# Optimization experiments

Measured on AMD Instinct MI355X. Metric: run time of the kernel, lower is better.

Reference implementation:

```python
import jax, jax.numpy as jnp
import numpy as np
import math

N_HEAD = 16
HEAD_QKV = 1024  # total qkv width; head_dim = HEAD_QKV // N_HEAD
WM_DECAY_LENGTH = 2048
WM_DECAY_RATE = 1.0
WM_ECHOIC = 16


def decay_weight_matrix(n):
    # power_law decay, faithful to get_decay_weight_matrix
    dl = WM_DECAY_LENGTH - WM_ECHOIC + 1
    nums = jnp.linspace(0.0, 1.0, dl)
    decay_values = 1.0 - jnp.power(nums, 1.0 / (np.e * WM_DECAY_RATE))
    decay_values = jnp.concatenate([jnp.ones(WM_ECHOIC - 1), decay_values])  # [WM_DECAY_LENGTH]
    decay_values = decay_values[:n]
    idx = jnp.arange(n)[:, None] - jnp.arange(n)[None, :]  # [n,n], negative above diag
    mat = decay_values[jnp.clip(idx, 0, n - 1)]
    return jnp.tril(mat).astype(jnp.float32)


def setup_inputs() -> dict:
    key = jax.random.key(0)
    k1, k2, k3 = jax.random.split(key, 3)
    B, T, C = 2, 2048, 1024
    x = jax.random.normal(k1, (B, T, C), dtype=jnp.float32)
    W_attn = jax.random.normal(k2, (C, 3 * HEAD_QKV), dtype=jnp.float32) * (1.0 / math.sqrt(C))
    W_proj = jax.random.normal(k3, (HEAD_QKV, C), dtype=jnp.float32) * (1.0 / math.sqrt(HEAD_QKV))
    return {"x": x, "W_attn": W_attn, "W_proj": W_proj}


def reference(x, W_attn, W_proj):
    B, T, C = x.shape
    hd = HEAD_QKV // N_HEAD
    qkv = x @ W_attn  # [B,T,3*HEAD_QKV]
    q, k, v = jnp.split(qkv, 3, axis=-1)
    # [B,T,HQKV] -> [B,H,T,hd]
    q = q.reshape(B, T, N_HEAD, hd).transpose(0, 2, 1, 3)
    k = k.reshape(B, T, N_HEAD, hd).transpose(0, 2, 1, 3)
    v = v.reshape(B, T, N_HEAD, hd).transpose(0, 2, 1, 3)
    att = jnp.einsum('bhqd,bhkd->bhqk', q, k) * (1.0 / math.sqrt(hd))
    causal = jnp.tril(jnp.ones((T, T), dtype=bool))
    att = jnp.where(causal, att, -jnp.inf)
    att = jax.nn.softmax(att, axis=-1)
    att = att * decay_weight_matrix(T)  # post-softmax multiplicative decay
    y = jnp.einsum('bhqk,bhkd->bhqd', att, v)
    y = y.transpose(0, 2, 1, 3).reshape(B, T, HEAD_QKV)
    return y @ W_proj
```

## Files before the change

kernel.cpp:

```cpp
#include <hip/hip_runtime.h>
#include <math.h>

#define B_  2
#define T_  2048
#define C_  1024
#define NH_ 16
#define HD_ 64
#define N3_ 3072

typedef float f32x4 __attribute__((ext_vector_type(4)));
typedef short bf16x8 __attribute__((ext_vector_type(8)));
typedef unsigned short u16;
typedef float f32x4_base __attribute__((ext_vector_type(4)));
typedef f32x4_base __attribute__((aligned(4))) f32x4u;

#define QSCALE 0.18033688011112042f

#if __has_builtin(__builtin_amdgcn_exp2f)
#define EXP2(x) __builtin_amdgcn_exp2f(x)
#else
#define EXP2(x) exp2f(x)
#endif

__device__ __forceinline__ u16 f2bf(float x) {
  unsigned int u = __builtin_bit_cast(unsigned int, x);
  u += 0x7FFFu + ((u >> 16) & 1u);
  return (u16)(u >> 16);
}

__device__ __forceinline__ unsigned int cvt_pk_bf16(float lo, float hi) {
  unsigned int r;
  asm("v_cvt_pk_bf16_f32 %0, %1, %2" : "=v"(r) : "v"(lo), "v"(hi));
  return r;
}

#define GLD16(g, l) __builtin_amdgcn_global_load_lds( \
    (__attribute__((address_space(1))) void*)(g), \
    (__attribute__((address_space(3))) void*)(l), 16, 0, 0)

__global__ __launch_bounds__(256) void cvt4_kernel(const float* __restrict__ in,
                                                   u16* __restrict__ out, int n) {
  int i = (blockIdx.x * 256 + threadIdx.x) * 4;
  if (i >= n) return;
  float4 v = *(const float4*)(in + i);
  ushort4 o;
  o.x = f2bf(v.x); o.y = f2bf(v.y); o.z = f2bf(v.z); o.w = f2bf(v.w);
  *(ushort4*)(out + i) = o;
}

__global__ __launch_bounds__(256) void transpose_cvt_kernel(const float* __restrict__ in,
                                                            u16* __restrict__ out,
                                                            int R, int Cc) {
  __shared__ float tile[32][33];
  int c0 = blockIdx.x * 32, r0 = blockIdx.y * 32;
  int tx = threadIdx.x & 31, ty = threadIdx.x >> 5;
#pragma unroll
  for (int rr = ty; rr < 32; rr += 8)
    tile[rr][tx] = in[(size_t)(r0 + rr) * Cc + c0 + tx];
  __syncthreads();
#pragma unroll
  for (int rr = ty; rr < 32; rr += 8)
    out[(size_t)(c0 + rr) * R + r0 + tx] = f2bf(tile[tx][rr]);
}

__global__ __launch_bounds__(256) void decay_init_kernel(float* __restrict__ decR) {
  int j = blockIdx.x * 256 + threadIdx.x;
  if (j >= 2176) return;
  int d = 2047 - j;
  float v = 1.0f;
  if (d >= 15) v = 1.0f - powf((float)(d - 15) * (1.0f / 2032.0f), 0.36787944117144233f);
  decR[j] = v;
}

__global__ __launch_bounds__(256) void vtrans_kernel(const u16* __restrict__ V,
                                                     u16* __restrict__ VT) {
  __shared__ u16 tile[64][72];
  int bh = blockIdx.y, t0 = blockIdx.x * 64;
  const u16* src = V + ((size_t)bh * T_ + t0) * HD_;
  int r = threadIdx.x >> 2;
  int c8 = (threadIdx.x & 3) * 16;
  *(bf16x8*)(&tile[r][c8])     = *(const bf16x8*)(src + (size_t)r * HD_ + c8);
  *(bf16x8*)(&tile[r][c8 + 8]) = *(const bf16x8*)(src + (size_t)r * HD_ + c8 + 8);
  __syncthreads();
  int d = threadIdx.x >> 2;
  int tc = (threadIdx.x & 3) * 16;
  u16 outv[16];
#pragma unroll
  for (int j = 0; j < 16; ++j) outv[j] = tile[tc + j][d];
  u16* dst = VT + ((size_t)bh * HD_ + d) * T_ + t0 + tc;
  *(bf16x8*)(dst)     = *(bf16x8*)(outv);
  *(bf16x8*)(dst + 8) = *(bf16x8*)(outv + 8);
}

template<int MODE>
__global__ __launch_bounds__(256, 3) void gemm128_kernel(
    const u16* __restrict__ A, const u16* __restrict__ Bt,
    float* __restrict__ Cf, u16* __restrict__ Cq, u16* __restrict__ Vt,
    int M, int N, int K)
{
  __shared__ char lds[32768];
  const int lane = threadIdx.x & 63;
  const int wave = threadIdx.x >> 6;
  const int nxb = N >> 7;
  const int orig = blockIdx.x;
  const int cpx = (int)gridDim.x >> 3;
  const int wg = (orig & 7) * cpx + (orig >> 3);
  const int m0 = (wg / nxb) << 7;
  const int n0 = (wg % nxb) << 7;
  const int wm = wave >> 1, wn = wave & 1;

  f32x4 acc[4][4] = {};

#define GSTAGE(buf, k0)                                                          \
  {                                                                              \
    _Pragma("unroll")                                                            \
    for (int c = 0; c < 2; ++c) {                                                \
      int chunk = wave * 2048 + c * 1024;                                        \
      int row = (chunk >> 6) + (lane >> 2);                                      \
      int wb = ((lane & 3) << 4) ^ ((row & 3) << 4);                             \
      GLD16((const char*)(A  + (size_t)(m0 + row) * K + (k0)) + wb,              \
            lds + (buf) * 16384 + chunk);                                        \
      GLD16((const char*)(Bt + (size_t)(n0 + row) * K + (k0)) + wb,              \
            lds + (buf) * 16384 + 8192 + chunk);                                 \
    }                                                                            \
  }

  GSTAGE(0, 0);
  __syncthreads();

  for (int k0 = 0; k0 < K; k0 += 32) {
    const int cur = (k0 >> 5) & 1;
    if (k0 + 32 < K) GSTAGE(cur ^ 1, k0 + 32);
    const char* base = lds + cur * 16384;
    bf16x8 af[4], bfr[4];
#pragma unroll
    for (int m = 0; m < 4; ++m) {
      int row = wm * 64 + m * 16 + (lane & 15);
      int wb = ((lane >> 4) << 4) ^ ((row & 3) << 4);
      af[m] = *(const bf16x8*)(base + row * 64 + wb);
    }
#pragma unroll
    for (int n = 0; n < 4; ++n) {
      int row = wn * 64 + n * 16 + (lane & 15);
      int wb = ((lane >> 4) << 4) ^ ((row & 3) << 4);
      bfr[n] = *(const bf16x8*)(base + 8192 + row * 64 + wb);
    }
    __builtin_amdgcn_s_setprio(1);
#pragma unroll
    for (int m = 0; m < 4; ++m)
#pragma unroll
      for (int n = 0; n < 4; ++n)
        acc[m][n] = __builtin_amdgcn_mfma_f32_16x16x32_bf16(af[m], bfr[n], acc[m][n], 0, 0, 0);
    __builtin_amdgcn_s_setprio(0);
    __syncthreads();
  }

#pragma unroll
  for (int m = 0; m < 4; ++m) {
    int grow0 = m0 + wm * 64 + m * 16 + ((lane >> 4) << 2);
#pragma unroll
    for (int n = 0; n < 4; ++n) {
      int gcol = n0 + wn * 64 + n * 16 + (lane & 15);
      f32x4 v = acc[m][n];
#pragma unroll
      for (int r = 0; r < 4; ++r) {
        int grow = grow0 + r;
        if (MODE == 0) {
          int bb = grow >> 11, tt = grow & 2047;
          int which = gcol >> 10, rem = gcol & 1023;
          int hh = rem >> 6, dd = rem & 63;
          if (which < 2) {
            float ov = (which == 0) ? v[r] * QSCALE : v[r];
            Cq[((size_t)(which * 32 + bb * 16 + hh) * 2048 + tt) * 64 + dd] = f2bf(ov);
          } else {
            Vt[((size_t)(bb * 16 + hh) * 2048 + tt) * 64 + dd] = f2bf(v[r]);
          }
        } else {
          Cf[(size_t)grow * N + gcol] = v[r];
        }
      }
    }
  }
#undef GSTAGE
}

__global__ __launch_bounds__(256, 3) void attn_kernel(
    const u16* __restrict__ qkb, const u16* __restrict__ vtg,
    const float* __restrict__ decR, u16* __restrict__ yb)
{
  __shared__ char klds[2][8192];
  __shared__ char vlds[2][8192];
  __shared__ u16 plds[128 * 76];

  const int lane = threadIdx.x & 63;
  const int wave = threadIdx.x >> 6;
  const int quad = lane >> 4;
  const int l15 = lane & 15;
  const int orig = blockIdx.x;
  const int wg = ((orig & 7) << 6) + (orig >> 3);
  const int qtA = wg & 15;
  const int qtB = 31 - qtA;
  const int bh = wg >> 4;
  const int b = bh >> 4, h = bh & 15;

  const u16* Q   = qkb + (size_t)bh * T_ * HD_;
  const u16* Kg  = qkb + (size_t)(32 + bh) * T_ * HD_;
  const u16* VTg = vtg + (size_t)bh * HD_ * T_;

  const int wrowB = qtB * 64 + wave * 16;
  const int wrowA = qtA * 64 + wave * 16;
  const int qB = wrowB + l15;
  const int qA = wrowA + l15;
  const int rbase0B = 2047 - qB + quad * 4;
  const int rbase0A = 2047 - qA + quad * 4;

  bf16x8 qaB[2], qaA[2];
  { const u16* qp = Q + (size_t)(wrowB + l15) * HD_ + quad * 8;
    qaB[0] = *(const bf16x8*)qp; qaB[1] = *(const bf16x8*)(qp + 32); }
  { const u16* qp = Q + (size_t)(wrowA + l15) * HD_ + quad * 8;
    qaA[0] = *(const bf16x8*)qp; qaA[1] = *(const bf16x8*)(qp + 32); }

  f32x4 accB[4] = {}, accA[4] = {};
  float lsumB = 0.0f, lsumA = 0.0f;

#define ASTAGE(buf, kt)                                                          \
  {                                                                              \
    _Pragma("unroll")                                                            \
    for (int c = 0; c < 2; ++c) {                                                \
      int chunk = wave * 2048 + c * 1024;                                        \
      int row = (chunk >> 7) + (lane >> 3);                                      \
      int wb = ((lane & 7) << 4) ^ ((row & 7) << 4);                             \
      GLD16((const char*)(Kg + (size_t)((kt) * 64 + row) * HD_) + wb,            \
            klds[buf] + chunk);                                                  \
      GLD16((const char*)(VTg + (size_t)row * T_ + (kt) * 64) + wb,              \
            vlds[buf] + chunk);                                                  \
    }                                                                            \
  }

  ASTAGE(0, 0);
  __syncthreads();

  const int nkt = qtB + 1;
  for (int kt = 0; kt < nkt; ++kt) {
    const int cur = kt & 1;
    if (kt + 1 < nkt) ASTAGE(cur ^ 1, kt + 1);
    const bool actA = (kt <= qtA);

    bf16x8 kf[4][2];
#pragma unroll
    for (int f = 0; f < 4; ++f) {
      int krow = f * 16 + l15;
      int base = krow * 128;
      int msk = (krow & 7) << 4;
      kf[f][0] = *(const bf16x8*)(klds[cur] + base + ((quad * 16) ^ msk));
      kf[f][1] = *(const bf16x8*)(klds[cur] + base + ((64 + quad * 16) ^ msk));
    }

    const float* dRB = decR + (rbase0B + kt * 64);
    const float* dRA = decR + (rbase0A + kt * 64);
    f32x4 dB[4], dA[4];
#pragma unroll
    for (int f = 0; f < 4; ++f) dB[f] = *(const f32x4u*)(dRB + f * 16);
    if (actA) {
#pragma unroll
      for (int f = 0; f < 4; ++f) dA[f] = *(const f32x4u*)(dRA + f * 16);
    }

    f32x4 sB[4], sA[4];
    __builtin_amdgcn_s_setprio(1);
#pragma unroll
    for (int f = 0; f < 4; ++f) {
      f32x4 t = {};
      t = __builtin_amdgcn_mfma_f32_16x16x32_bf16(kf[f][0], qaB[0], t, 0, 0, 0);
      t = __builtin_amdgcn_mfma_f32_16x16x32_bf16(kf[f][1], qaB[1], t, 0, 0, 0);
      sB[f] = t;
    }
    if (actA) {
#pragma unroll
      for (int f = 0; f < 4; ++f) {
        f32x4 t = {};
        t = __builtin_amdgcn_mfma_f32_16x16x32_bf16(kf[f][0], qaA[0], t, 0, 0, 0);
        t = __builtin_amdgcn_mfma_f32_16x16x32_bf16(kf[f][1], qaA[1], t, 0, 0, 0);
        sA[f] = t;
      }
    }
    __builtin_amdgcn_s_setprio(0);

    if (kt == qtB) {
#pragma unroll
      for (int f = 0; f < 4; ++f) {
        int key0 = kt * 64 + f * 16 + quad * 4;
#pragma unroll
        for (int r = 0; r < 4; ++r)
          if (key0 + r > qB) sB[f][r] = -1e30f;
      }
    }
    if (actA && kt == qtA) {
#pragma unroll
      for (int f = 0; f < 4; ++f) {
        int key0 = kt * 64 + f * 16 + quad * 4;
#pragma unroll
        for (int r = 0; r < 4; ++r)
          if (key0 + r > qA) sA[f][r] = -1e30f;
      }
    }

#pragma unroll
    for (int f = 0; f < 4; ++f) {
      f32x4 p;
#pragma unroll
      for (int r = 0; r < 4; ++r) p[r] = EXP2(sB[f][r]);
      lsumB += (p[0] + p[1]) + (p[2] + p[3]);
      unsigned int w0 = cvt_pk_bf16(p[0] * dB[f][0], p[1] * dB[f][1]);
      unsigned int w1 = cvt_pk_bf16(p[2] * dB[f][2], p[3] * dB[f][3]);
      uint2 wv; wv.x = w0; wv.y = w1;
      *(uint2*)(plds + (size_t)(wave * 16 + l15) * 76 + f * 16 + quad * 4) = wv;
    }
    if (actA) {
#pragma unroll
      for (int f = 0; f < 4; ++f) {
        f32x4 p;
#pragma unroll
        for (int r = 0; r < 4; ++r) p[r] = EXP2(sA[f][r]);
        lsumA += (p[0] + p[1]) + (p[2] + p[3]);
        unsigned int w0 = cvt_pk_bf16(p[0] * dA[f][0], p[1] * dA[f][1]);
        unsigned int w1 = cvt_pk_bf16(p[2] * dA[f][2], p[3] * dA[f][3]);
        uint2 wv; wv.x = w0; wv.y = w1;
        *(uint2*)(plds + (size_t)(64 + wave * 16 + l15) * 76 + f * 16 + quad * 4) = wv;
      }
    }

    bf16x8 vf[4][2];
#pragma unroll
    for (int n = 0; n < 4; ++n) {
      int vrow = n * 16 + l15;
      int mskv = (vrow & 7) << 4;
#pragma unroll
      for (int ks = 0; ks < 2; ++ks)
        vf[n][ks] = *(const bf16x8*)(vlds[cur] + vrow * 128 + ((ks * 64 + quad * 16) ^ mskv));
    }

    __builtin_amdgcn_s_setprio(1);
#pragma unroll
    for (int ks = 0; ks < 2; ++ks) {
      bf16x8 pa = *(const bf16x8*)(plds + (size_t)(wave * 16 + l15) * 76 + ks * 32 + quad * 8);
#pragma unroll
      for (int n = 0; n < 4; ++n)
        accB[n] = __builtin_amdgcn_mfma_f32_16x16x32_bf16(pa, vf[n][ks], accB[n], 0, 0, 0);
    }
    if (actA) {
#pragma unroll
      for (int ks = 0; ks < 2; ++ks) {
        bf16x8 pa = *(const bf16x8*)(plds + (size_t)(64 + wave * 16 + l15) * 76 + ks * 32 + quad * 8);
#pragma unroll
        for (int n = 0; n < 4; ++n)
          accA[n] = __builtin_amdgcn_mfma_f32_16x16x32_bf16(pa, vf[n][ks], accA[n], 0, 0, 0);
      }
    }
    __builtin_amdgcn_s_setprio(0);
    __syncthreads();
  }
#undef ASTAGE

  lsumB += __shfl_xor(lsumB, 16); lsumB += __shfl_xor(lsumB, 32);
  lsumA += __shfl_xor(lsumA, 16); lsumA += __shfl_xor(lsumA, 32);
  float rB[4], rA[4];
#pragma unroll
  for (int r = 0; r < 4; ++r) {
    rB[r] = 1.0f / __shfl(lsumB, quad * 4 + r, 16);
    rA[r] = 1.0f / __shfl(lsumA, quad * 4 + r, 16);
  }
#pragma unroll
  for (int n = 0; n < 4; ++n) {
    int d = h * 64 + n * 16 + l15;
#pragma unroll
    for (int r = 0; r < 4; ++r) {
      int tB = wrowB + quad * 4 + r;
      int tA = wrowA + quad * 4 + r;
      yb[((size_t)b * T_ + tB) * 1024 + d] = f2bf(accB[n][r] * rB[r]);
      yb[((size_t)b * T_ + tA) * 1024 + d] = f2bf(accA[n][r] * rA[r]);
    }
  }
}

extern "C" void kernel_launch(void* const* d_in, const int* in_sizes, int n_in,
                              void* d_out, int out_size, void* d_ws, size_t ws_size,
                              hipStream_t stream) {
  const float* x  = (const float*)d_in[0];
  const float* Wa = (const float*)d_in[1];
  const float* Wp = (const float*)d_in[2];
  float* out = (float*)d_out;
  char* ws = (char*)d_ws;

  u16*   xb    = (u16*)(ws + 0);
  u16*   WaT   = (u16*)(ws + 8388608);
  u16*   WpT   = (u16*)(ws + 14680064);
  u16*   qkb   = (u16*)(ws + 16777216);
  u16*   Vtmp  = (u16*)(ws + 33554432);
  u16*   VT    = (u16*)(ws + 41943040);
  float* decR  = (float*)Vtmp;
  u16*   yb    = xb;

  cvt4_kernel<<<4096, 256, 0, stream>>>(x, xb, B_ * T_ * C_);
  transpose_cvt_kernel<<<dim3(96, 32), 256, 0, stream>>>(Wa, WaT, C_, N3_);
  transpose_cvt_kernel<<<dim3(32, 32), 256, 0, stream>>>(Wp, WpT, C_, C_);

  gemm128_kernel<0><<<768, 256, 0, stream>>>(
      xb, WaT, nullptr, qkb, Vtmp, B_ * T_, N3_, C_);
  vtrans_kernel<<<dim3(32, 32), 256, 0, stream>>>(Vtmp, VT);
  decay_init_kernel<<<9, 256, 0, stream>>>(decR);
  attn_kernel<<<512, 256, 0, stream>>>(qkb, VT, decR, yb);
  gemm128_kernel<1><<<256, 256, 0, stream>>>(
      yb, WpT, out, nullptr, nullptr, B_ * T_, 1024, 1024);
}
```

Before: 120.7 us.

## Fuse prep kernels, triple-buffer GEMM, write V transposed, prefetch decay in attention

Combines the x conversion, both weight transposes and the decay table init into one prep kernel, and drops the separate V transpose kernel by having the QKV GEMM epilogue write V directly in transposed layout. The GEMM moves to a three-stage LDS pipeline with explicit vmcnt waits and one barrier per iteration. Attention prefetches the next tile's decay factors into registers, replaces the trailing syncthreads with a barrier at loop top, remaps blocks so heads stay grouped per XCD with balanced query tiles, and lowers launch bounds to 2 waves. This cuts launch count and global round trips but raises LDS and register use, which lowers GEMM occupancy.

```diff
diff --git a/kernel.cpp b/kernel.cpp
--- a/kernel.cpp
+++ b/kernel.cpp
@@ -38,58 +38,49 @@
     (__attribute__((address_space(1))) void*)(g), \
     (__attribute__((address_space(3))) void*)(l), 16, 0, 0)
 
-__global__ __launch_bounds__(256) void cvt4_kernel(const float* __restrict__ in,
-                                                   u16* __restrict__ out, int n) {
-  int i = (blockIdx.x * 256 + threadIdx.x) * 4;
-  if (i >= n) return;
-  float4 v = *(const float4*)(in + i);
-  ushort4 o;
-  o.x = f2bf(v.x); o.y = f2bf(v.y); o.z = f2bf(v.z); o.w = f2bf(v.w);
-  *(ushort4*)(out + i) = o;
-}
-
-__global__ __launch_bounds__(256) void transpose_cvt_kernel(const float* __restrict__ in,
-                                                            u16* __restrict__ out,
-                                                            int R, int Cc) {
+__global__ __launch_bounds__(256) void prep_kernel(
+    const float* __restrict__ x, u16* __restrict__ xb,
+    const float* __restrict__ Wa, u16* __restrict__ WaT,
+    const float* __restrict__ Wp, u16* __restrict__ WpT,
+    float* __restrict__ decR)
+{
   __shared__ float tile[32][33];
-  int c0 = blockIdx.x * 32, r0 = blockIdx.y * 32;
-  int tx = threadIdx.x & 31, ty = threadIdx.x >> 5;
-#pragma unroll
-  for (int rr = ty; rr < 32; rr += 8)
-    tile[rr][tx] = in[(size_t)(r0 + rr) * Cc + c0 + tx];
-  __syncthreads();
-#pragma unroll
-  for (int rr = ty; rr < 32; rr += 8)
-    out[(size_t)(c0 + rr) * R + r0 + tx] = f2bf(tile[tx][rr]);
-}
-
-__global__ __launch_bounds__(256) void decay_init_kernel(float* __restrict__ decR) {
-  int j = blockIdx.x * 256 + threadIdx.x;
-  if (j >= 2176) return;
-  int d = 2047 - j;
-  float v = 1.0f;
-  if (d >= 15) v = 1.0f - powf((float)(d - 15) * (1.0f / 2032.0f), 0.36787944117144233f);
-  decR[j] = v;
-}
-
-__global__ __launch_bounds__(256) void vtrans_kernel(const u16* __restrict__ V,
-                                                     u16* __restrict__ VT) {
-  __shared__ u16 tile[64][72];
-  int bh = blockIdx.y, t0 = blockIdx.x * 64;
-  const u16* src = V + ((size_t)bh * T_ + t0) * HD_;
-  int r = threadIdx.x >> 2;
-  int c8 = (threadIdx.x & 3) * 16;
-  *(bf16x8*)(&tile[r][c8])     = *(const bf16x8*)(src + (size_t)r * HD_ + c8);
-  *(bf16x8*)(&tile[r][c8 + 8]) = *(const bf16x8*)(src + (size_t)r * HD_ + c8 + 8);
-  __syncthreads();
-  int d = threadIdx.x >> 2;
-  int tc = (threadIdx.x & 3) * 16;
-  u16 outv[16];
-#pragma unroll
-  for (int j = 0; j < 16; ++j) outv[j] = tile[tc + j][d];
-  u16* dst = VT + ((size_t)bh * HD_ + d) * T_ + t0 + tc;
-  *(bf16x8*)(dst)     = *(bf16x8*)(outv);
-  *(bf16x8*)(dst + 8) = *(bf16x8*)(outv + 8);
+  const int bid = blockIdx.x;
+  const int tid = threadIdx.x;
+  if (bid < 4096) {
+    int i = (bid * 256 + tid) * 4;
+    float4 v = *(const float4*)(x + i);
+    ushort4 o;
+    o.x = f2bf(v.x); o.y = f2bf(v.y); o.z = f2bf(v.z); o.w = f2bf(v.w);
+    *(ushort4*)(xb + i) = o;
+  } else if (bid < 8192) {
+    const float* in; u16* out; int Cc, c0, r0;
+    if (bid < 7168) {
+      int t = bid - 4096;
+      in = Wa; out = WaT; Cc = N3_;
+      c0 = (t % 96) * 32; r0 = (t / 96) * 32;
+    } else {
+      int t = bid - 7168;
+      in = Wp; out = WpT; Cc = C_;
+      c0 = (t % 32) * 32; r0 = (t / 32) * 32;
+    }
+    int tx = tid & 31, ty = tid >> 5;
+#pragma unroll
+    for (int rr = ty; rr < 32; rr += 8)
+      tile[rr][tx] = in[(size_t)(r0 + rr) * Cc + c0 + tx];
+    __syncthreads();
+#pragma unroll
+    for (int rr = ty; rr < 32; rr += 8)
+      out[(size_t)(c0 + rr) * 1024 + r0 + tx] = f2bf(tile[tx][rr]);
+  } else {
+    int j = (bid - 8192) * 256 + tid;
+    if (j < 4352) {
+      int d = 2047 - j;
+      float v = 1.0f;
+      if (d >= 15) v = 1.0f - powf((float)(d - 15) * (1.0f / 2032.0f), 0.36787944117144233f);
+      decR[j] = v;
+    }
+  }
 }
 
 template<int MODE>
@@ -98,7 +89,7 @@
     float* __restrict__ Cf, u16* __restrict__ Cq, u16* __restrict__ Vt,
     int M, int N, int K)
 {
-  __shared__ char lds[32768];
+  __shared__ char lds[49152];
   const int lane = threadIdx.x & 63;
   const int wave = threadIdx.x >> 6;
   const int nxb = N >> 7;
@@ -125,13 +116,19 @@
     }                                                                            \
   }
 
+  const int nk = K >> 5;
   GSTAGE(0, 0);
+  GSTAGE(1, 32);
   __syncthreads();
 
-  for (int k0 = 0; k0 < K; k0 += 32) {
-    const int cur = (k0 >> 5) & 1;
-    if (k0 + 32 < K) GSTAGE(cur ^ 1, k0 + 32);
-    const char* base = lds + cur * 16384;
+  for (int i = 0; i < nk; ++i) {
+    if (i + 1 < nk) asm volatile("s_waitcnt vmcnt(4)" ::: "memory");
+    else            asm volatile("s_waitcnt vmcnt(0)" ::: "memory");
+    __builtin_amdgcn_s_barrier();
+    __builtin_amdgcn_sched_barrier(0);
+    if (i + 2 < nk) GSTAGE((i + 2) % 3, (i + 2) * 32);
+
+    const char* base = lds + (i % 3) * 16384;
     bf16x8 af[4], bfr[4];
 #pragma unroll
     for (int m = 0; m < 4; ++m) {
@@ -152,7 +149,6 @@
       for (int n = 0; n < 4; ++n)
         acc[m][n] = __builtin_amdgcn_mfma_f32_16x16x32_bf16(af[m], bfr[n], acc[m][n], 0, 0, 0);
     __builtin_amdgcn_s_setprio(0);
-    __syncthreads();
   }
 
 #pragma unroll
@@ -162,29 +158,32 @@
     for (int n = 0; n < 4; ++n) {
       int gcol = n0 + wn * 64 + n * 16 + (lane & 15);
       f32x4 v = acc[m][n];
-#pragma unroll
-      for (int r = 0; r < 4; ++r) {
-        int grow = grow0 + r;
-        if (MODE == 0) {
-          int bb = grow >> 11, tt = grow & 2047;
-          int which = gcol >> 10, rem = gcol & 1023;
-          int hh = rem >> 6, dd = rem & 63;
-          if (which < 2) {
+      if (MODE == 0) {
+        int bb = grow0 >> 11, tt0 = grow0 & 2047;
+        int which = gcol >> 10, rem = gcol & 1023;
+        int hh = rem >> 6, dd = rem & 63;
+        if (which < 2) {
+#pragma unroll
+          for (int r = 0; r < 4; ++r) {
             float ov = (which == 0) ? v[r] * QSCALE : v[r];
-            Cq[((size_t)(which * 32 + bb * 16 + hh) * 2048 + tt) * 64 + dd] = f2bf(ov);
-          } else {
-            Vt[((size_t)(bb * 16 + hh) * 2048 + tt) * 64 + dd] = f2bf(v[r]);
+            Cq[((size_t)(which * 32 + bb * 16 + hh) * 2048 + tt0 + r) * 64 + dd] = f2bf(ov);
           }
         } else {
-          Cf[(size_t)grow * N + gcol] = v[r];
+          ushort4 o;
+          o.x = f2bf(v[0]); o.y = f2bf(v[1]); o.z = f2bf(v[2]); o.w = f2bf(v[3]);
+          *(ushort4*)(Vt + ((size_t)(bb * 16 + hh) * 64 + dd) * 2048 + tt0) = o;
         }
+      } else {
+#pragma unroll
+        for (int r = 0; r < 4; ++r)
+          Cf[(size_t)(grow0 + r) * N + gcol] = v[r];
       }
     }
   }
 #undef GSTAGE
 }
 
-__global__ __launch_bounds__(256, 3) void attn_kernel(
+__global__ __launch_bounds__(256, 2) void attn_kernel(
     const u16* __restrict__ qkb, const u16* __restrict__ vtg,
     const float* __restrict__ decR, u16* __restrict__ yb)
 {
@@ -197,10 +196,12 @@
   const int quad = lane >> 4;
   const int l15 = lane & 15;
   const int orig = blockIdx.x;
-  const int wg = ((orig & 7) << 6) + (orig >> 3);
-  const int qtA = wg & 15;
+  const int xcd = orig & 7;
+  const int j = orig >> 3;
+  const int bh = xcd * 4 + (j & 3);
+  const int tt = j >> 2;
+  const int qtA = (tt < 8) ? tt : 23 - tt;
   const int qtB = 31 - qtA;
-  const int bh = wg >> 4;
   const int b = bh >> 4, h = bh & 15;
 
   const u16* Q   = qkb + (size_t)bh * T_ * HD_;
@@ -211,13 +212,13 @@
   const int wrowA = qtA * 64 + wave * 16;
   const int qB = wrowB + l15;
   const int qA = wrowA + l15;
-  const int rbase0B = 2047 - qB + quad * 4;
-  const int rbase0A = 2047 - qA + quad * 4;
+  const float* dpB = decR + (2047 - qB + quad * 4);
+  const float* dpA = decR + (2047 - qA + quad * 4);
 
   bf16x8 qaB[2], qaA[2];
-  { const u16* qp = Q + (size_t)(wrowB + l15) * HD_ + quad * 8;
+  { const u16* qp = Q + (size_t)qB * HD_ + quad * 8;
     qaB[0] = *(const bf16x8*)qp; qaB[1] = *(const bf16x8*)(qp + 32); }
-  { const u16* qp = Q + (size_t)(wrowA + l15) * HD_ + quad * 8;
+  { const u16* qp = Q + (size_t)qA * HD_ + quad * 8;
     qaA[0] = *(const bf16x8*)qp; qaA[1] = *(const bf16x8*)(qp + 32); }
 
   f32x4 accB[4] = {}, accA[4] = {};
@@ -237,13 +238,32 @@
     }                                                                            \
   }
 
+  f32x4 dBc[4], dAc[4], dBn[4], dAn[4];
+#pragma unroll
+  for (int f = 0; f < 4; ++f) {
+    dBn[f] = *(const f32x4u*)(dpB + f * 16);
+    dAn[f] = *(const f32x4u*)(dpA + f * 16);
+  }
   ASTAGE(0, 0);
   __syncthreads();
 
   const int nkt = qtB + 1;
   for (int kt = 0; kt < nkt; ++kt) {
     const int cur = kt & 1;
+#pragma unroll
+    for (int f = 0; f < 4; ++f) { dBc[f] = dBn[f]; dAc[f] = dAn[f]; }
+    const float* dB1 = dpB + (kt + 1) * 64;
+    const float* dA1 = dpA + (kt + 1) * 64;
+#pragma unroll
+    for (int f = 0; f < 4; ++f) {
+      dBn[f] = *(const f32x4u*)(dB1 + f * 16);
+      dAn[f] = *(const f32x4u*)(dA1 + f * 16);
+    }
+    asm volatile("s_waitcnt vmcnt(8)" ::: "memory");
+    __builtin_amdgcn_s_barrier();
+    __builtin_amdgcn_sched_barrier(0);
     if (kt + 1 < nkt) ASTAGE(cur ^ 1, kt + 1);
+
     const bool actA = (kt <= qtA);
 
     bf16x8 kf[4][2];
@@ -256,16 +276,6 @@
       kf[f][1] = *(const bf16x8*)(klds[cur] + base + ((64 + quad * 16) ^ msk));
     }
 
-    const float* dRB = decR + (rbase0B + kt * 64);
-    const float* dRA = decR + (rbase0A + kt * 64);
-    f32x4 dB[4], dA[4];
-#pragma unroll
-    for (int f = 0; f < 4; ++f) dB[f] = *(const f32x4u*)(dRB + f * 16);
-    if (actA) {
-#pragma unroll
-      for (int f = 0; f < 4; ++f) dA[f] = *(const f32x4u*)(dRA + f * 16);
-    }
-
     f32x4 sB[4], sA[4];
     __builtin_amdgcn_s_setprio(1);
 #pragma unroll
@@ -311,8 +321,8 @@
 #pragma unroll
       for (int r = 0; r < 4; ++r) p[r] = EXP2(sB[f][r]);
       lsumB += (p[0] + p[1]) + (p[2] + p[3]);
-      unsigned int w0 = cvt_pk_bf16(p[0] * dB[f][0], p[1] * dB[f][1]);
-      unsigned int w1 = cvt_pk_bf16(p[2] * dB[f][2], p[3] * dB[f][3]);
+      unsigned int w0 = cvt_pk_bf16(p[0] * dBc[f][0], p[1] * dBc[f][1]);
+      unsigned int w1 = cvt_pk_bf16(p[2] * dBc[f][2], p[3] * dBc[f][3]);
       uint2 wv; wv.x = w0; wv.y = w1;
       *(uint2*)(plds + (size_t)(wave * 16 + l15) * 76 + f * 16 + quad * 4) = wv;
     }
@@ -323,8 +333,8 @@
 #pragma unroll
         for (int r = 0; r < 4; ++r) p[r] = EXP2(sA[f][r]);
         lsumA += (p[0] + p[1]) + (p[2] + p[3]);
-        unsigned int w0 = cvt_pk_bf16(p[0] * dA[f][0], p[1] * dA[f][1]);
-        unsigned int w1 = cvt_pk_bf16(p[2] * dA[f][2], p[3] * dA[f][3]);
+        unsigned int w0 = cvt_pk_bf16(p[0] * dAc[f][0], p[1] * dAc[f][1]);
+        unsigned int w1 = cvt_pk_bf16(p[2] * dAc[f][2], p[3] * dAc[f][3]);
         uint2 wv; wv.x = w0; wv.y = w1;
         *(uint2*)(plds + (size_t)(64 + wave * 16 + l15) * 76 + f * 16 + quad * 4) = wv;
       }
@@ -358,7 +368,6 @@
       }
     }
     __builtin_amdgcn_s_setprio(0);
-    __syncthreads();
   }
 #undef ASTAGE
 
@@ -396,19 +405,13 @@
   u16*   WaT   = (u16*)(ws + 8388608);
   u16*   WpT   = (u16*)(ws + 14680064);
   u16*   qkb   = (u16*)(ws + 16777216);
-  u16*   Vtmp  = (u16*)(ws + 33554432);
+  float* decR  = (float*)(ws + 33554432);
   u16*   VT    = (u16*)(ws + 41943040);
-  float* decR  = (float*)Vtmp;
   u16*   yb    = xb;
 
-  cvt4_kernel<<<4096, 256, 0, stream>>>(x, xb, B_ * T_ * C_);
-  transpose_cvt_kernel<<<dim3(96, 32), 256, 0, stream>>>(Wa, WaT, C_, N3_);
-  transpose_cvt_kernel<<<dim3(32, 32), 256, 0, stream>>>(Wp, WpT, C_, C_);
-
+  prep_kernel<<<8209, 256, 0, stream>>>(x, xb, Wa, WaT, Wp, WpT, decR);
   gemm128_kernel<0><<<768, 256, 0, stream>>>(
-      xb, WaT, nullptr, qkb, Vtmp, B_ * T_, N3_, C_);
-  vtrans_kernel<<<dim3(32, 32), 256, 0, stream>>>(Vtmp, VT);
-  decay_init_kernel<<<9, 256, 0, stream>>>(decR);
+      xb, WaT, nullptr, qkb, VT, B_ * T_, N3_, C_);
   attn_kernel<<<512, 256, 0, stream>>>(qkb, VT, decR, yb);
   gemm128_kernel<1><<<256, 256, 0, stream>>>(
       yb, WpT, out, nullptr, nullptr, B_ * T_, 1024, 1024);
```

After: 104.5 us. 13.4% less time.
